# Optimization experiments

Measured on AMD Instinct MI355X. Metric: run time of the kernel, lower is better.

Reference implementation:

```python
import jax, jax.numpy as jnp
import numpy as np

N, E = 50000, 800000
NFEAT, NHID = 128, 128


def setup_inputs() -> dict:
    key = jax.random.key(0)
    ks = jax.random.split(key, 10)
    s = 1.0 / np.sqrt(NFEAT)
    inp = {
        "x": jax.random.normal(ks[0], (N, NFEAT), dtype=jnp.float32),
        "edge_index": jax.random.randint(ks[1], (2, E), 0, N, dtype=jnp.int32),
        "head": 0,
        # Relation params (nn.Linear weights, [out, in], bias=False)
        "gamma1_w": jax.random.uniform(ks[2], (NFEAT, NFEAT), jnp.float32, -s, s),
        "gamma2_w": jax.random.uniform(ks[3], (NFEAT, NFEAT), jnp.float32, -s, s),
        "beta1_w": jax.random.uniform(ks[4], (NFEAT, NFEAT), jnp.float32, -s, s),
        "beta2_w": jax.random.uniform(ks[5], (NFEAT, NFEAT), jnp.float32, -s, s),
        "r": jax.random.uniform(ks[6], (1, NFEAT), jnp.float32, -s, s),
        # GCNConv params: lin (bias=False) + conv bias
        "lin_w": jax.random.uniform(ks[7], (NHID, NFEAT), jnp.float32, -s, s),
        "bias": jnp.zeros((NHID,), dtype=jnp.float32),
    }
    return inp


def _lrelu(v):
    return jnp.where(v >= 0, v, 0.2 * v)  # LeakyReLU(0.2)


def _forward(x, edge_index, gamma1_w, gamma2_w, beta1_w, beta2_w, r, lin_w, bias):
    n = x.shape[0]
    row, col = edge_index[0], edge_index[1]
    ones_e = jnp.ones((edge_index.shape[1],), dtype=x.dtype)

    # num_neighbor = scatter_add(ones, row); neighbor = scatter_mean(x[col], row)
    num_neighbor = jax.ops.segment_sum(ones_e, row, num_segments=n)  # [N]
    neigh_sum = jax.ops.segment_sum(x[col], row, num_segments=n)      # [N, F]
    neighbor = neigh_sum / jnp.maximum(num_neighbor, 1.0)[:, None]

    # Relation (ablation=0): FiLM-style translation vector
    gamma = _lrelu(x @ gamma1_w.T + neighbor @ gamma2_w.T) + 1.0
    beta = _lrelu(x @ beta1_w.T + neighbor @ beta2_w.T)
    output = x + (gamma * r + beta) - neighbor                        # [N, F]

    xw = x @ lin_w.T                                                  # [N, H]
    loop = jnp.arange(n, dtype=row.dtype)
    row2 = jnp.concatenate([row, loop])
    col2 = jnp.concatenate([col, loop])
    deg = jax.ops.segment_sum(jnp.ones_like(row2, dtype=x.dtype), col2, num_segments=n)
    dinv = jnp.where(deg > 0, jax.lax.rsqrt(deg), 0.0)
    norm = dinv[row2] * dinv[col2]                                    # [E+N]
    h_k = jax.ops.segment_sum(norm[:, None] * xw[row2], col2, num_segments=n) + bias

    # tail branch (head=False, ablation=0): h_s = output, projected by gc.lin.weight
    h_s = output @ lin_w.T
    h_k = (h_k + h_s) / (num_neighbor + 1.0)[:, None]
    return h_k, output


def reference(x, edge_index, head, gamma1_w, gamma2_w, beta1_w, beta2_w, r, lin_w, bias):
    # head is a static Python int (0 -> tail branch, the full fused path)
    assert not head
    return _forward(x, edge_index, gamma1_w, gamma2_w, beta1_w, beta2_w, r, lin_w, bias)
```

## Files before the change

### kernel.cpp

```cpp
#include <hip/hip_runtime.h>

#define NN 50000
#define NE 800000
#define NF 128

#define SHIFT 8
#define NB 196
#define PBLOCKS 128
#define PCHUNK ((NE + PBLOCKS - 1) / PBLOCKS)

#define NTILES ((NN + 63) / 64)
#define FBLOCKS 512

typedef __attribute__((ext_vector_type(4))) float f32x4;
typedef __attribute__((ext_vector_type(8))) short bf16x8;

__device__ __forceinline__ short f2bf(float f) {
    unsigned u = __float_as_uint(f);
    u += 0x7FFF + ((u >> 16) & 1);
    return (short)(u >> 16);
}
__device__ __forceinline__ float bf2f(short s) {
    return __uint_as_float(((unsigned)(unsigned short)s) << 16);
}

__global__ __launch_bounds__(256) void p0_count_kernel(const int* __restrict__ ei,
                                                       int* __restrict__ gcnt) {
    __shared__ int cnt[2 * NB];
    int t = threadIdx.x;
    for (int i = t; i < 2 * NB; i += 256) cnt[i] = 0;
    __syncthreads();
    int lo = blockIdx.x * PCHUNK;
    int hi = min(lo + PCHUNK, NE);
    for (int j = lo + t; j < hi; j += 256) {
        int r = ei[j];
        int c = ei[NE + j];
        atomicAdd(&cnt[r >> SHIFT], 1);
        atomicAdd(&cnt[NB + (c >> SHIFT)], 1);
    }
    __syncthreads();
    for (int i = t; i < 2 * NB; i += 256)
        if (cnt[i]) atomicAdd(&gcnt[i], cnt[i]);
}

__global__ __launch_bounds__(256) void p1_scan_kernel(const int* __restrict__ gcnt,
                                                      int* __restrict__ baseR,
                                                      int* __restrict__ baseC,
                                                      int* __restrict__ gcur) {
    __shared__ int s[256];
    int t = threadIdx.x;
    int v = (t < NB) ? gcnt[t] : 0;
    s[t] = v;
    __syncthreads();
    for (int off = 1; off < 256; off <<= 1) {
        int u = (t >= off) ? s[t - off] : 0;
        __syncthreads();
        s[t] += u;
        __syncthreads();
    }
    if (t < NB) {
        int excl = s[t] - v;
        baseR[t] = excl;
        gcur[t] = excl;
        if (t == NB - 1) baseR[NB] = s[t];
    }
    __syncthreads();
    int v2 = (t < NB) ? gcnt[NB + t] : 0;
    s[t] = v2;
    __syncthreads();
    for (int off = 1; off < 256; off <<= 1) {
        int u = (t >= off) ? s[t - off] : 0;
        __syncthreads();
        s[t] += u;
        __syncthreads();
    }
    if (t < NB) {
        int excl = s[t] - v2;
        baseC[t] = excl;
        gcur[NB + t] = excl;
        if (t == NB - 1) baseC[NB] = s[t];
    }
}

__global__ __launch_bounds__(256) void p2_partition_kernel(const int* __restrict__ ei,
                                                           int* __restrict__ gcur,
                                                           unsigned* __restrict__ partR,
                                                           unsigned* __restrict__ partC) {
    __shared__ int cnt[2 * NB];
    __shared__ int res[2 * NB];
    int t = threadIdx.x;
    for (int i = t; i < 2 * NB; i += 256) cnt[i] = 0;
    __syncthreads();
    int lo = blockIdx.x * PCHUNK;
    int hi = min(lo + PCHUNK, NE);
    for (int j = lo + t; j < hi; j += 256) {
        int r = ei[j];
        int c = ei[NE + j];
        atomicAdd(&cnt[r >> SHIFT], 1);
        atomicAdd(&cnt[NB + (c >> SHIFT)], 1);
    }
    __syncthreads();
    for (int i = t; i < 2 * NB; i += 256) {
        int n = cnt[i];
        res[i] = n ? atomicAdd(&gcur[i], n) : 0;
        cnt[i] = 0;
    }
    __syncthreads();
    for (int j = lo + t; j < hi; j += 256) {
        int r = ei[j];
        int c = ei[NE + j];
        int bR = r >> SHIFT;
        int sR = atomicAdd(&cnt[bR], 1);
        partR[res[bR] + sR] = ((unsigned)(r & 255) << 17) | (unsigned)c;
        int bC = NB + (c >> SHIFT);
        int sC = atomicAdd(&cnt[bC], 1);
        partC[res[bC] + sC] = ((unsigned)(c & 255) << 17) | (unsigned)r;
    }
}

__global__ __launch_bounds__(256) void p3_build_kernel(
    const unsigned* __restrict__ partR, const unsigned* __restrict__ partC,
    const int* __restrict__ baseR, const int* __restrict__ baseC,
    int* __restrict__ offs_r, int* __restrict__ offs_c,
    int* __restrict__ csr_r, int* __restrict__ csr_c,
    int* __restrict__ degr, float* __restrict__ dinv) {
    int side = blockIdx.x / NB;
    int b = blockIdx.x - side * NB;
    const unsigned* part = side ? partC : partR;
    const int* base = side ? baseC : baseR;
    int* offs = side ? offs_c : offs_r;
    int* csr = side ? csr_c : csr_r;

    __shared__ int deg[256];
    __shared__ int cur[256];
    int t = threadIdx.x;
    int s0 = base[b], s1 = base[b + 1];
    deg[t] = 0;
    __syncthreads();
    for (int j = s0 + t; j < s1; j += 256)
        atomicAdd(&deg[part[j] >> 17], 1);
    __syncthreads();
    int myDeg = deg[t];
    for (int off = 1; off < 256; off <<= 1) {
        int u = (t >= off) ? deg[t - off] : 0;
        __syncthreads();
        deg[t] += u;
        __syncthreads();
    }
    int excl = deg[t] - myDeg;
    int node = (b << SHIFT) + t;
    if (node <= NN) offs[node] = s0 + excl;
    if (node < NN) {
        if (side == 0) degr[node] = myDeg;
        else           dinv[node] = rsqrtf((float)myDeg + 1.0f);
    }
    cur[t] = excl;
    __syncthreads();
    for (int j = s0 + t; j < s1; j += 256) {
        unsigned en = part[j];
        int k = en >> 17;
        int p = atomicAdd(&cur[k], 1);
        csr[s0 + p] = (int)(en & 0x1FFFFu);
    }
}

__global__ void convert_x_kernel(const float* __restrict__ x, short* __restrict__ xbf) {
    int i = blockIdx.x * blockDim.x + threadIdx.x;
    if (i >= NN * NF / 8) return;
    float4 a = ((const float4*)x)[i * 2];
    float4 b = ((const float4*)x)[i * 2 + 1];
    bf16x8 v;
    v[0] = f2bf(a.x); v[1] = f2bf(a.y); v[2] = f2bf(a.z); v[3] = f2bf(a.w);
    v[4] = f2bf(b.x); v[5] = f2bf(b.y); v[6] = f2bf(b.z); v[7] = f2bf(b.w);
    *(bf16x8*)(xbf + i * 8) = v;
}

__global__ void convert_w_kernel(const float* __restrict__ g1, const float* __restrict__ g2,
                                 const float* __restrict__ b1, const float* __restrict__ b2,
                                 const float* __restrict__ lin, short* __restrict__ wbf) {
    int i = blockIdx.x * blockDim.x + threadIdx.x;
    if (i >= 5 * NF * NF) return;
    int m = i >> 14, off = i & (NF * NF - 1);
    float v = (m == 0) ? g1[off] : (m == 1) ? g2[off] : (m == 2) ? b1[off]
            : (m == 3) ? b2[off] : lin[off];
    wbf[i] = f2bf(v);
}

__global__ __launch_bounds__(256) void gather_fused_kernel(
    const int* __restrict__ offs_r, const int* __restrict__ csr_r,
    const int* __restrict__ offs_c, const int* __restrict__ csr_c,
    const short* __restrict__ xbf, const float* __restrict__ dinv,
    short* __restrict__ nbbf, short* __restrict__ zbf) {
    int g = blockIdx.x * 16 + (threadIdx.x >> 4);
    int l = threadIdx.x & 15;
    if (g >= NN) return;
    const short* xb = xbf + l * 8;

    int s = offs_r[g], e = offs_r[g + 1];
    float acc[8] = {0.f, 0.f, 0.f, 0.f, 0.f, 0.f, 0.f, 0.f};
    int j = s;
    for (; j + 2 <= e; j += 2) {
        int s0 = csr_r[j], s1 = csr_r[j + 1];
        bf16x8 v0 = *(const bf16x8*)(xb + s0 * NF);
        bf16x8 v1 = *(const bf16x8*)(xb + s1 * NF);
        #pragma unroll
        for (int k = 0; k < 8; ++k) acc[k] += bf2f(v0[k]) + bf2f(v1[k]);
    }
    if (j < e) {
        bf16x8 v = *(const bf16x8*)(xb + csr_r[j] * NF);
        #pragma unroll
        for (int k = 0; k < 8; ++k) acc[k] += bf2f(v[k]);
    }
    float invn = 1.0f / fmaxf((float)(e - s), 1.0f);
    bf16x8 o;
    #pragma unroll
    for (int k = 0; k < 8; ++k) o[k] = f2bf(acc[k] * invn);
    *(bf16x8*)(nbbf + g * NF + l * 8) = o;

    s = offs_c[g]; e = offs_c[g + 1];
    float az[8] = {0.f, 0.f, 0.f, 0.f, 0.f, 0.f, 0.f, 0.f};
    j = s;
    for (; j + 2 <= e; j += 2) {
        int s0 = csr_c[j], s1 = csr_c[j + 1];
        float w0 = dinv[s0], w1 = dinv[s1];
        bf16x8 v0 = *(const bf16x8*)(xb + s0 * NF);
        bf16x8 v1 = *(const bf16x8*)(xb + s1 * NF);
        #pragma unroll
        for (int k = 0; k < 8; ++k) az[k] += w0 * bf2f(v0[k]) + w1 * bf2f(v1[k]);
    }
    if (j < e) {
        int s0 = csr_c[j];
        float w0 = dinv[s0];
        bf16x8 v = *(const bf16x8*)(xb + s0 * NF);
        #pragma unroll
        for (int k = 0; k < 8; ++k) az[k] += w0 * bf2f(v[k]);
    }
    float dc = dinv[g];
    bf16x8 self = *(const bf16x8*)(xb + g * NF);
    bf16x8 zo;
    #pragma unroll
    for (int k = 0; k < 8; ++k) zo[k] = f2bf(dc * (az[k] + dc * bf2f(self[k])));
    *(bf16x8*)(zbf + g * NF + l * 8) = zo;
}

__global__ __launch_bounds__(256, 2) void film_mfma_kernel(
    const short* __restrict__ xbf, const short* __restrict__ nbbf,
    const short* __restrict__ zbf, const short* __restrict__ wbf,
    const float* __restrict__ rvec, const float* __restrict__ bias,
    const int* __restrict__ degr, float* __restrict__ outp,
    float* __restrict__ hko) {
    __shared__ short xs[64 * NF];
    __shared__ short ns[64 * NF];
    __shared__ short zs[64 * NF];

    int tid = threadIdx.x;
    int w = tid >> 6;
    int l = tid & 63;
    int lr = l & 15;
    int lg = l >> 4;

    bf16x8 wf[2][5][4];
    float rc[2], bc[2];
    #pragma unroll
    for (int j = 0; j < 2; ++j) {
        int col = (2 * w + j) * 16 + lr;
        #pragma unroll
        for (int m = 0; m < 5; ++m) {
            const short* wm = wbf + m * 16384 + col * NF;
            #pragma unroll
            for (int kb = 0; kb < 4; ++kb)
                wf[j][m][kb] = *(const bf16x8*)(wm + kb * 32 + lg * 8);
        }
        rc[j] = rvec[col];
        bc[j] = bias[col];
    }

    #pragma unroll 1
    for (int tile = blockIdx.x; tile < NTILES; tile += FBLOCKS) {
        int node0 = tile * 64;

        #pragma unroll
        for (int it = 0; it < 4; ++it) {
            int chunk = it * 256 + tid;
            int row = chunk >> 4;
            int c = chunk & 15;
            int grow = min(node0 + row, NN - 1);
            int swz = ((c ^ (row & 7)) << 3);
            *(bf16x8*)(xs + row * NF + swz) = *(const bf16x8*)(xbf + grow * NF + c * 8);
            *(bf16x8*)(ns + row * NF + swz) = *(const bf16x8*)(nbbf + grow * NF + c * 8);
            *(bf16x8*)(zs + row * NF + swz) = *(const bf16x8*)(zbf + grow * NF + c * 8);
        }
        __syncthreads();

        #pragma unroll 1
        for (int rg = 0; rg < 4; ++rg) {
            bf16x8 xf[4], nf[4];
            #pragma unroll
            for (int kb = 0; kb < 4; ++kb) {
                int row = rg * 16 + lr;
                int swz = (((kb * 4 + lg) ^ (row & 7)) << 3);
                xf[kb] = *(const bf16x8*)(xs + row * NF + swz);
                nf[kb] = *(const bf16x8*)(ns + row * NF + swz);
            }
            #pragma unroll
            for (int j = 0; j < 2; ++j) {
                f32x4 ag = {0.f, 0.f, 0.f, 0.f};
                f32x4 ab = {0.f, 0.f, 0.f, 0.f};
                #pragma unroll
                for (int kb = 0; kb < 4; ++kb) {
                    ag = __builtin_amdgcn_mfma_f32_16x16x32_bf16(xf[kb], wf[j][0][kb], ag, 0, 0, 0);
                    ag = __builtin_amdgcn_mfma_f32_16x16x32_bf16(nf[kb], wf[j][1][kb], ag, 0, 0, 0);
                    ab = __builtin_amdgcn_mfma_f32_16x16x32_bf16(xf[kb], wf[j][2][kb], ab, 0, 0, 0);
                    ab = __builtin_amdgcn_mfma_f32_16x16x32_bf16(nf[kb], wf[j][3][kb], ab, 0, 0, 0);
                }
                int col = (2 * w + j) * 16 + lr;
                #pragma unroll
                for (int q = 0; q < 4; ++q) {
                    int nl = rg * 16 + lg * 4 + q;
                    int ng = node0 + nl;
                    int addr = nl * NF + (((col >> 3) ^ (nl & 7)) << 3) + (col & 7);
                    float xv = bf2f(xs[addr]);
                    float nv = bf2f(ns[addr]);
                    float gp = ag[q], bp = ab[q];
                    float gamma = (gp >= 0.f ? gp : 0.2f * gp) + 1.0f;
                    float beta  = (bp >= 0.f ? bp : 0.2f * bp);
                    float o = xv + gamma * rc[j] + beta - nv;
                    if (ng < NN) outp[ng * NF + col] = o;
                    zs[addr] = f2bf(o + bf2f(zs[addr]));
                }
            }
        }
        __syncthreads();

        #pragma unroll 1
        for (int rg = 0; rg < 4; ++rg) {
            bf16x8 of[4];
            #pragma unroll
            for (int kb = 0; kb < 4; ++kb) {
                int row = rg * 16 + lr;
                int swz = (((kb * 4 + lg) ^ (row & 7)) << 3);
                of[kb] = *(const bf16x8*)(zs + row * NF + swz);
            }
            float invdq[4];
            #pragma unroll
            for (int q = 0; q < 4; ++q)
                invdq[q] = 1.0f / ((float)degr[min(node0 + rg * 16 + lg * 4 + q, NN - 1)] + 1.0f);
            #pragma unroll
            for (int j = 0; j < 2; ++j) {
                f32x4 as = {0.f, 0.f, 0.f, 0.f};
                #pragma unroll
                for (int kb = 0; kb < 4; ++kb)
                    as = __builtin_amdgcn_mfma_f32_16x16x32_bf16(of[kb], wf[j][4][kb], as, 0, 0, 0);
                int col = (2 * w + j) * 16 + lr;
                #pragma unroll
                for (int q = 0; q < 4; ++q) {
                    int ng = node0 + rg * 16 + lg * 4 + q;
                    if (ng < NN) hko[ng * NF + col] = (as[q] + bc[j]) * invdq[q];
                }
            }
        }
        __syncthreads();
    }
}

extern "C" void kernel_launch(void* const* d_in, const int* in_sizes, int n_in,
                              void* d_out, int out_size, void* d_ws, size_t ws_size,
                              hipStream_t stream) {
    const float* x    = (const float*)d_in[0];
    const int*   ei   = (const int*)d_in[1];
    const float* g1   = (const float*)d_in[3];
    const float* g2   = (const float*)d_in[4];
    const float* b1   = (const float*)d_in[5];
    const float* b2   = (const float*)d_in[6];
    const float* rv   = (const float*)d_in[7];
    const float* lin  = (const float*)d_in[8];
    const float* bias = (const float*)d_in[9];

    float* dinv = (float*)d_ws;
    int* degr   = (int*)(dinv + NN);
    int* offs_r = degr + NN;
    int* offs_c = offs_r + (NN + 1);
    int* csr_r  = offs_c + (NN + 1);
    int* csr_c  = csr_r + NE;
    unsigned* partR = (unsigned*)(csr_c + NE);
    unsigned* partC = partR + NE;
    int* gcnt   = (int*)(partC + NE);
    int* gcur   = gcnt + 2 * NB;
    int* baseR  = gcur + 2 * NB;
    int* baseC  = baseR + (NB + 1);
    uintptr_t p = (uintptr_t)(baseC + NB + 1);
    p = (p + 15) & ~(uintptr_t)15;
    short* xbf  = (short*)p;
    short* nbbf = xbf + NN * NF;
    short* zbf  = nbbf + NN * NF;
    short* wbf  = zbf + NN * NF;

    float* hko  = (float*)d_out;
    float* outp = hko + NN * NF;

    hipMemsetAsync(gcnt, 0, 2 * NB * sizeof(int), stream);

    p0_count_kernel<<<PBLOCKS, 256, 0, stream>>>(ei, gcnt);
    p1_scan_kernel<<<1, 256, 0, stream>>>(gcnt, baseR, baseC, gcur);
    p2_partition_kernel<<<PBLOCKS, 256, 0, stream>>>(ei, gcur, partR, partC);
    p3_build_kernel<<<2 * NB, 256, 0, stream>>>(partR, partC, baseR, baseC,
                                                offs_r, offs_c, csr_r, csr_c, degr, dinv);
    convert_x_kernel<<<(NN * NF / 8 + 255) / 256, 256, 0, stream>>>(x, xbf);
    convert_w_kernel<<<(5 * NF * NF + 255) / 256, 256, 0, stream>>>(g1, g2, b1, b2, lin, wbf);
    gather_fused_kernel<<<(NN + 15) / 16, 256, 0, stream>>>(offs_r, csr_r, offs_c, csr_c,
                                                            xbf, dinv, nbbf, zbf);
    film_mfma_kernel<<<FBLOCKS, 256, 0, stream>>>(xbf, nbbf, zbf, wbf, rv, bias, degr,
                                                  outp, hko);
}
```

Measured before the change: 175.2 us.

## Merge conversion kernels into count kernel and unroll gather loops by four

The x and weight bf16 conversion kernels are folded into the edge-count kernel as extra block ranges, so one launch does all three jobs and the conversions run alongside the counting instead of as separate serialized launches. The neighbor gather loops in the fused gather kernel are unrolled from two to four edges per iteration, which puts more independent row loads in flight to hide memory latency. The unrolling raises register pressure, and merging the launches mixes blocks that do different amounts of work.

```diff
diff --git a/kernel.cpp b/kernel.cpp
--- a/kernel.cpp
+++ b/kernel.cpp
@@ -12,6 +12,10 @@
 #define NTILES ((NN + 63) / 64)
 #define FBLOCKS 512
 
+#define CVX_BLOCKS 3125
+#define CVW_BLOCKS 320
+#define PREP_BLOCKS (CVX_BLOCKS + CVW_BLOCKS + PBLOCKS)
+
 typedef __attribute__((ext_vector_type(4))) float f32x4;
 typedef __attribute__((ext_vector_type(8))) short bf16x8;
 
@@ -24,13 +28,42 @@
     return __uint_as_float(((unsigned)(unsigned short)s) << 16);
 }
 
-__global__ __launch_bounds__(256) void p0_count_kernel(const int* __restrict__ ei,
-                                                       int* __restrict__ gcnt) {
+__global__ __launch_bounds__(256) void prep_kernel(
+    const float* __restrict__ x, const float* __restrict__ g1,
+    const float* __restrict__ g2, const float* __restrict__ b1,
+    const float* __restrict__ b2, const float* __restrict__ lin,
+    const int* __restrict__ ei, short* __restrict__ xbf,
+    short* __restrict__ wbf, int* __restrict__ gcnt) {
     __shared__ int cnt[2 * NB];
+    int bid = blockIdx.x;
     int t = threadIdx.x;
+
+    if (bid < CVX_BLOCKS) {
+        int i = bid * 256 + t;
+        if (i < NN * NF / 8) {
+            float4 a = ((const float4*)x)[i * 2];
+            float4 b = ((const float4*)x)[i * 2 + 1];
+            bf16x8 v;
+            v[0] = f2bf(a.x); v[1] = f2bf(a.y); v[2] = f2bf(a.z); v[3] = f2bf(a.w);
+            v[4] = f2bf(b.x); v[5] = f2bf(b.y); v[6] = f2bf(b.z); v[7] = f2bf(b.w);
+            *(bf16x8*)(xbf + i * 8) = v;
+        }
+        return;
+    }
+    if (bid < CVX_BLOCKS + CVW_BLOCKS) {
+        int i = (bid - CVX_BLOCKS) * 256 + t;
+        if (i < 5 * NF * NF) {
+            int m = i >> 14, off = i & (NF * NF - 1);
+            float v = (m == 0) ? g1[off] : (m == 1) ? g2[off] : (m == 2) ? b1[off]
+                    : (m == 3) ? b2[off] : lin[off];
+            wbf[i] = f2bf(v);
+        }
+        return;
+    }
+    int pb = bid - CVX_BLOCKS - CVW_BLOCKS;
     for (int i = t; i < 2 * NB; i += 256) cnt[i] = 0;
     __syncthreads();
-    int lo = blockIdx.x * PCHUNK;
+    int lo = pb * PCHUNK;
     int hi = min(lo + PCHUNK, NE);
     for (int j = lo + t; j < hi; j += 256) {
         int r = ei[j];
@@ -164,28 +197,6 @@
     }
 }
 
-__global__ void convert_x_kernel(const float* __restrict__ x, short* __restrict__ xbf) {
-    int i = blockIdx.x * blockDim.x + threadIdx.x;
-    if (i >= NN * NF / 8) return;
-    float4 a = ((const float4*)x)[i * 2];
-    float4 b = ((const float4*)x)[i * 2 + 1];
-    bf16x8 v;
-    v[0] = f2bf(a.x); v[1] = f2bf(a.y); v[2] = f2bf(a.z); v[3] = f2bf(a.w);
-    v[4] = f2bf(b.x); v[5] = f2bf(b.y); v[6] = f2bf(b.z); v[7] = f2bf(b.w);
-    *(bf16x8*)(xbf + i * 8) = v;
-}
-
-__global__ void convert_w_kernel(const float* __restrict__ g1, const float* __restrict__ g2,
-                                 const float* __restrict__ b1, const float* __restrict__ b2,
-                                 const float* __restrict__ lin, short* __restrict__ wbf) {
-    int i = blockIdx.x * blockDim.x + threadIdx.x;
-    if (i >= 5 * NF * NF) return;
-    int m = i >> 14, off = i & (NF * NF - 1);
-    float v = (m == 0) ? g1[off] : (m == 1) ? g2[off] : (m == 2) ? b1[off]
-            : (m == 3) ? b2[off] : lin[off];
-    wbf[i] = f2bf(v);
-}
-
 __global__ __launch_bounds__(256) void gather_fused_kernel(
     const int* __restrict__ offs_r, const int* __restrict__ csr_r,
     const int* __restrict__ offs_c, const int* __restrict__ csr_c,
@@ -199,14 +210,17 @@
     int s = offs_r[g], e = offs_r[g + 1];
     float acc[8] = {0.f, 0.f, 0.f, 0.f, 0.f, 0.f, 0.f, 0.f};
     int j = s;
-    for (; j + 2 <= e; j += 2) {
-        int s0 = csr_r[j], s1 = csr_r[j + 1];
+    for (; j + 4 <= e; j += 4) {
+        int s0 = csr_r[j], s1 = csr_r[j + 1], s2 = csr_r[j + 2], s3 = csr_r[j + 3];
         bf16x8 v0 = *(const bf16x8*)(xb + s0 * NF);
         bf16x8 v1 = *(const bf16x8*)(xb + s1 * NF);
-        #pragma unroll
-        for (int k = 0; k < 8; ++k) acc[k] += bf2f(v0[k]) + bf2f(v1[k]);
-    }
-    if (j < e) {
+        bf16x8 v2 = *(const bf16x8*)(xb + s2 * NF);
+        bf16x8 v3 = *(const bf16x8*)(xb + s3 * NF);
+        #pragma unroll
+        for (int k = 0; k < 8; ++k)
+            acc[k] += (bf2f(v0[k]) + bf2f(v1[k])) + (bf2f(v2[k]) + bf2f(v3[k]));
+    }
+    for (; j < e; ++j) {
         bf16x8 v = *(const bf16x8*)(xb + csr_r[j] * NF);
         #pragma unroll
         for (int k = 0; k < 8; ++k) acc[k] += bf2f(v[k]);
@@ -220,15 +234,19 @@
     s = offs_c[g]; e = offs_c[g + 1];
     float az[8] = {0.f, 0.f, 0.f, 0.f, 0.f, 0.f, 0.f, 0.f};
     j = s;
-    for (; j + 2 <= e; j += 2) {
-        int s0 = csr_c[j], s1 = csr_c[j + 1];
-        float w0 = dinv[s0], w1 = dinv[s1];
+    for (; j + 4 <= e; j += 4) {
+        int s0 = csr_c[j], s1 = csr_c[j + 1], s2 = csr_c[j + 2], s3 = csr_c[j + 3];
+        float w0 = dinv[s0], w1 = dinv[s1], w2 = dinv[s2], w3 = dinv[s3];
         bf16x8 v0 = *(const bf16x8*)(xb + s0 * NF);
         bf16x8 v1 = *(const bf16x8*)(xb + s1 * NF);
-        #pragma unroll
-        for (int k = 0; k < 8; ++k) az[k] += w0 * bf2f(v0[k]) + w1 * bf2f(v1[k]);
-    }
-    if (j < e) {
+        bf16x8 v2 = *(const bf16x8*)(xb + s2 * NF);
+        bf16x8 v3 = *(const bf16x8*)(xb + s3 * NF);
+        #pragma unroll
+        for (int k = 0; k < 8; ++k)
+            az[k] += (w0 * bf2f(v0[k]) + w1 * bf2f(v1[k]))
+                   + (w2 * bf2f(v2[k]) + w3 * bf2f(v3[k]));
+    }
+    for (; j < e; ++j) {
         int s0 = csr_c[j];
         float w0 = dinv[s0];
         bf16x8 v = *(const bf16x8*)(xb + s0 * NF);
@@ -400,13 +418,12 @@
 
     hipMemsetAsync(gcnt, 0, 2 * NB * sizeof(int), stream);
 
-    p0_count_kernel<<<PBLOCKS, 256, 0, stream>>>(ei, gcnt);
+    prep_kernel<<<PREP_BLOCKS, 256, 0, stream>>>(x, g1, g2, b1, b2, lin, ei,
+                                                 xbf, wbf, gcnt);
     p1_scan_kernel<<<1, 256, 0, stream>>>(gcnt, baseR, baseC, gcur);
     p2_partition_kernel<<<PBLOCKS, 256, 0, stream>>>(ei, gcur, partR, partC);
     p3_build_kernel<<<2 * NB, 256, 0, stream>>>(partR, partC, baseR, baseC,
                                                 offs_r, offs_c, csr_r, csr_c, degr, dinv);
-    convert_x_kernel<<<(NN * NF / 8 + 255) / 256, 256, 0, stream>>>(x, xbf);
-    convert_w_kernel<<<(5 * NF * NF + 255) / 256, 256, 0, stream>>>(g1, g2, b1, b2, lin, wbf);
     gather_fused_kernel<<<(NN + 15) / 16, 256, 0, stream>>>(offs_r, csr_r, offs_c, csr_c,
                                                             xbf, dinv, nbbf, zbf);
     film_mfma_kernel<<<FBLOCKS, 256, 0, stream>>>(xbf, nbbf, zbf, wbf, rv, bias, degr,
```

Result: no change. 173.8 us (-0.8%).
